# Kernel tuning notes

Hardware: AMD Instinct MI355X
Metric: run time of the kernel (lower is better)

## Reference

```python
import jax, jax.numpy as jnp
import numpy as np
from jax import lax

B, C, H, W = 64, 256, 64, 64
RED = 16


def setup_inputs() -> dict:
    key = jax.random.key(0)
    k1, k2, k3, k4, k5 = jax.random.split(key, 5)
    x = jax.random.normal(k1, (B, C, H, W), dtype=jnp.float32)
    # conv1: Conv2d(C, 1, kernel_size=1) -> weight (1,C,1,1) stored squeezed as (C,), bias scalar
    conv_w = jax.random.normal(k2, (C,), dtype=jnp.float32) * (1.0 / np.sqrt(C))
    conv_b = jax.random.normal(k3, (1,), dtype=jnp.float32) * 0.01
    # SE MLP: Linear(C, C//RED, bias=False), Linear(C//RED, C, bias=False)
    fc1_w = jax.random.normal(k4, (C // RED, C), dtype=jnp.float32) * (1.0 / np.sqrt(C))
    fc2_w = jax.random.normal(k5, (C, C // RED), dtype=jnp.float32) * (1.0 / np.sqrt(C // RED))
    return {"x": x, "conv_w": conv_w, "conv_b": conv_b, "fc1_w": fc1_w, "fc2_w": fc2_w}


def reference(x, conv_w, conv_b, fc1_w, fc2_w):
    b, c, h, w = x.shape
    # --- spatial_pool ---
    # group batch into chunks of 8, pool over (group, H, W) with 3x3x3 avg, stride 1, pad 1
    g = x.reshape(b // 8, 8, c, h, w).transpose(0, 2, 1, 3, 4)  # (G, C, 8, H, W)
    summed = lax.reduce_window(
        g, 0.0, lax.add,
        window_dimensions=(1, 1, 3, 3, 3),
        window_strides=(1, 1, 1, 1, 1),
        padding=[(0, 0), (0, 0), (1, 1), (1, 1), (1, 1)],
    )
    pooled = summed / 27.0  # AvgPool3d(3,1,1) with count_include_pad=True
    pooled = pooled.transpose(0, 2, 1, 3, 4).reshape(b, c, h, w)
    # 1x1 conv C -> 1
    logits = jnp.einsum('bchw,c->bhw', pooled, conv_w) + conv_b[0]  # (B,H,W)
    attn = jax.nn.softmax(logits.reshape(b, h * w), axis=-1)  # softmax over spatial positions
    # softmax-weighted spatial pooling of the ORIGINAL x
    y = jnp.einsum('bcs,bs->bc', x.reshape(b, c, h * w), attn)  # (B,C)
    # --- SE gating MLP ---
    hid = jax.nn.relu(y @ fc1_w.T)           # (B, C//RED)
    gate = jax.nn.sigmoid(hid @ fc2_w.T)     # (B, C)
    return x * gate[:, :, None, None]
```

## Files before the change

### kernel.cpp

```cpp
#include <hip/hip_runtime.h>
#include <math.h>

#define B 64
#define C 256
#define S 4096
#define S4 1024

__global__ __launch_bounds__(256) void k1_chanreduce(const float4* __restrict__ x4,
                                                     const float* __restrict__ cw,
                                                     float4* __restrict__ t4) {
    __shared__ float wl[C];
    const int tid = threadIdx.x;
    wl[tid] = cw[tid];
    __syncthreads();
    const int b = blockIdx.x >> 2;
    const int chunk = blockIdx.x & 3;
    const int s4 = chunk * 256 + tid;
    const float4* xb = x4 + (size_t)b * C * S4 + s4;
    float4 acc = make_float4(0.f, 0.f, 0.f, 0.f);
#pragma unroll 8
    for (int c = 0; c < C; ++c) {
        float4 v = xb[(size_t)c * S4];
        float w = wl[c];
        acc.x += v.x * w; acc.y += v.y * w; acc.z += v.z * w; acc.w += v.w * w;
    }
    t4[b * S4 + s4] = acc;
}

__global__ __launch_bounds__(256) void k2_pool_softmax(const float* __restrict__ t,
                                                       const float* __restrict__ cb,
                                                       float* __restrict__ attn) {
    __shared__ float ts[S];
    __shared__ float rs[S];
    __shared__ float red[16];
    const int b = blockIdx.x;
    const int d = b & 7;
    const int tid = threadIdx.x;
    const float* t0 = t + (size_t)b * S;

    for (int k = 0; k < 16; ++k) {
        int s = k * 256 + tid;
        float v = t0[s];
        if (d > 0) v += t0[s - S];
        if (d < 7) v += t0[s + S];
        ts[s] = v;
    }
    __syncthreads();
    for (int k = 0; k < 16; ++k) {
        int s = k * 256 + tid;
        int w = s & 63;
        float v = ts[s];
        if (w > 0)  v += ts[s - 1];
        if (w < 63) v += ts[s + 1];
        rs[s] = v;
    }
    __syncthreads();
    const float bias = cb[0];
    float l[16];
    float m = -INFINITY;
    for (int k = 0; k < 16; ++k) {
        int s = k * 256 + tid;
        float v = rs[s];
        if (s >= 64)     v += rs[s - 64];
        if (s < S - 64)  v += rs[s + 64];
        l[k] = v * (1.0f / 27.0f) + bias;
        m = fmaxf(m, l[k]);
    }
    for (int o = 32; o > 0; o >>= 1) m = fmaxf(m, __shfl_xor(m, o));
    const int wave = tid >> 6;
    if ((tid & 63) == 0) red[wave] = m;
    __syncthreads();
    if (tid == 0) {
        float mm = red[0];
        for (int i = 1; i < 4; ++i) mm = fmaxf(mm, red[i]);
        red[8] = mm;
    }
    __syncthreads();
    m = red[8];
    float sum = 0.f;
    for (int k = 0; k < 16; ++k) { l[k] = expf(l[k] - m); sum += l[k]; }
    for (int o = 32; o > 0; o >>= 1) sum += __shfl_xor(sum, o);
    if ((tid & 63) == 0) red[wave] = sum;
    __syncthreads();
    if (tid == 0) {
        float ss = red[0] + red[1] + red[2] + red[3];
        red[9] = 1.0f / ss;
    }
    __syncthreads();
    const float inv = red[9];
    float* ab = attn + (size_t)b * S;
    for (int k = 0; k < 16; ++k) {
        int s = k * 256 + tid;
        ab[s] = l[k] * inv;
    }
}

__global__ __launch_bounds__(256) void k3_weighted_pool(const float4* __restrict__ x4,
                                                        const float4* __restrict__ attn4,
                                                        float* __restrict__ y) {
    __shared__ float4 al[S4];
    const int tid = threadIdx.x;
    const int b = blockIdx.x >> 6;
    const int cg = blockIdx.x & 63;
    for (int k = 0; k < 4; ++k) {
        int i = k * 256 + tid;
        al[i] = attn4[(size_t)b * S4 + i];
    }
    __syncthreads();
    const int c = cg * 4 + (tid >> 6);
    const int lane = tid & 63;
    const float4* xb = x4 + ((size_t)(b * C + c)) * S4;
    float acc = 0.f;
#pragma unroll 4
    for (int it = 0; it < 16; ++it) {
        int s4 = it * 64 + lane;
        float4 xv = xb[s4];
        float4 av = al[s4];
        acc += xv.x * av.x + xv.y * av.y + xv.z * av.z + xv.w * av.w;
    }
    for (int o = 32; o > 0; o >>= 1) acc += __shfl_xor(acc, o);
    if (lane == 0) y[b * C + c] = acc;
}

__global__ __launch_bounds__(256) void k4_mlp(const float* __restrict__ y,
                                              const float* __restrict__ fc1,
                                              const float* __restrict__ fc2,
                                              float* __restrict__ gate) {
    __shared__ float yl[C];
    __shared__ float ph[16][17];
    __shared__ float hid[16];
    const int b = blockIdx.x;
    const int tid = threadIdx.x;
    yl[tid] = y[(size_t)b * C + tid];
    __syncthreads();
    const int j = tid >> 4, part = tid & 15;
    float p = 0.f;
#pragma unroll
    for (int k = 0; k < 16; ++k) {
        int cc = part + k * 16;
        p += yl[cc] * fc1[j * C + cc];
    }
    ph[j][part] = p;
    __syncthreads();
    if (tid < 16) {
        float s = 0.f;
#pragma unroll
        for (int k = 0; k < 16; ++k) s += ph[tid][k];
        hid[tid] = fmaxf(s, 0.f);
    }
    __syncthreads();
    float g = 0.f;
#pragma unroll
    for (int jj = 0; jj < 16; ++jj) g += hid[jj] * fc2[tid * 16 + jj];
    gate[(size_t)b * C + tid] = 1.0f / (1.0f + expf(-g));
}

__global__ __launch_bounds__(256) void k5_scale(const float4* __restrict__ x4,
                                               const float* __restrict__ gate,
                                               float4* __restrict__ out4) {
    const size_t total = (size_t)B * C * S4;
    size_t i = (size_t)blockIdx.x * 256 + threadIdx.x;
    const size_t stride = (size_t)gridDim.x * 256;
    for (; i < total; i += stride) {
        int bc = (int)(i >> 10);
        float g = gate[bc];
        float4 v = x4[i];
        v.x *= g; v.y *= g; v.z *= g; v.w *= g;
        out4[i] = v;
    }
}

extern "C" void kernel_launch(void* const* d_in, const int* in_sizes, int n_in,
                              void* d_out, int out_size, void* d_ws, size_t ws_size,
                              hipStream_t stream) {
    const float* x   = (const float*)d_in[0];
    const float* cw  = (const float*)d_in[1];
    const float* cb  = (const float*)d_in[2];
    const float* fc1 = (const float*)d_in[3];
    const float* fc2 = (const float*)d_in[4];
    float* out = (float*)d_out;

    float* t    = (float*)d_ws;
    float* attn = t + (size_t)B * S;
    float* y    = attn + (size_t)B * S;
    float* gate = y + (size_t)B * C;

    k1_chanreduce<<<256, 256, 0, stream>>>((const float4*)x, cw, (float4*)t);
    k2_pool_softmax<<<B, 256, 0, stream>>>(t, cb, attn);
    k3_weighted_pool<<<B * 64, 256, 0, stream>>>((const float4*)x, (const float4*)attn, y);
    k4_mlp<<<B, 256, 0, stream>>>(y, fc1, fc2, gate);
    k5_scale<<<4096, 256, 0, stream>>>((const float4*)x, gate, (float4*)out);
}
```

Before: 546.7 us.

## Fuse SE MLP into scale kernel, split channel reduce, reverse k3 batch order

The channel-reduction kernel now runs 1024 blocks: four waves each reduce 64 channels and the partial sums are combined through shared memory. The weighted-pool kernel drops its shared-memory staging of attention and walks batches in reverse order, presumably to hit data k2/k1 left in cache. The SE MLP is fused into the scale kernel, so each of 1024 blocks recomputes the gate for its batch, and x/out use nontemporal loads and stores. This removes one launch and the gate round trip, and adds occupancy to k1. In exchange the MLP work is repeated 16 times per batch.

Result: faster. 533.8 us (-2.4%).

```diff
diff --git a/kernel.cpp b/kernel.cpp
--- a/kernel.cpp
+++ b/kernel.cpp
@@ -6,25 +6,37 @@
 #define S 4096
 #define S4 1024
 
+typedef float v4f __attribute__((ext_vector_type(4)));
+
 __global__ __launch_bounds__(256) void k1_chanreduce(const float4* __restrict__ x4,
                                                      const float* __restrict__ cw,
                                                      float4* __restrict__ t4) {
-    __shared__ float wl[C];
-    const int tid = threadIdx.x;
-    wl[tid] = cw[tid];
-    __syncthreads();
-    const int b = blockIdx.x >> 2;
-    const int chunk = blockIdx.x & 3;
-    const int s4 = chunk * 256 + tid;
-    const float4* xb = x4 + (size_t)b * C * S4 + s4;
+    __shared__ float4 sh[256];
+    const int tid = threadIdx.x;
+    const int b = blockIdx.x >> 4;
+    const int chunk = blockIdx.x & 15;
+    const int cg = tid >> 6;
+    const int s4i = tid & 63;
+    const int s4 = chunk * 64 + s4i;
+    const float4* xb = x4 + (size_t)b * C * S4 + (size_t)cg * 64 * S4 + s4;
     float4 acc = make_float4(0.f, 0.f, 0.f, 0.f);
 #pragma unroll 8
-    for (int c = 0; c < C; ++c) {
-        float4 v = xb[(size_t)c * S4];
-        float w = wl[c];
+    for (int k = 0; k < 64; ++k) {
+        float4 v = xb[(size_t)k * S4];
+        float w = cw[cg * 64 + k];
         acc.x += v.x * w; acc.y += v.y * w; acc.z += v.z * w; acc.w += v.w * w;
     }
-    t4[b * S4 + s4] = acc;
+    sh[tid] = acc;
+    __syncthreads();
+    if (cg == 0) {
+        float4 a = sh[s4i], b2 = sh[64 + s4i], c2 = sh[128 + s4i], d2 = sh[192 + s4i];
+        float4 r;
+        r.x = a.x + b2.x + c2.x + d2.x;
+        r.y = a.y + b2.y + c2.y + d2.y;
+        r.z = a.z + b2.z + c2.z + d2.z;
+        r.w = a.w + b2.w + c2.w + d2.w;
+        t4[(size_t)b * S4 + s4] = r;
+    }
 }
 
 __global__ __launch_bounds__(256) void k2_pool_softmax(const float* __restrict__ t,
@@ -98,49 +110,51 @@
 __global__ __launch_bounds__(256) void k3_weighted_pool(const float4* __restrict__ x4,
                                                         const float4* __restrict__ attn4,
                                                         float* __restrict__ y) {
-    __shared__ float4 al[S4];
-    const int tid = threadIdx.x;
-    const int b = blockIdx.x >> 6;
+    const int tid = threadIdx.x;
+    const int b = (B - 1) - (blockIdx.x >> 6);
     const int cg = blockIdx.x & 63;
-    for (int k = 0; k < 4; ++k) {
-        int i = k * 256 + tid;
-        al[i] = attn4[(size_t)b * S4 + i];
-    }
-    __syncthreads();
     const int c = cg * 4 + (tid >> 6);
     const int lane = tid & 63;
     const float4* xb = x4 + ((size_t)(b * C + c)) * S4;
+    const float4* ab = attn4 + (size_t)b * S4;
     float acc = 0.f;
 #pragma unroll 4
     for (int it = 0; it < 16; ++it) {
         int s4 = it * 64 + lane;
         float4 xv = xb[s4];
-        float4 av = al[s4];
+        float4 av = ab[s4];
         acc += xv.x * av.x + xv.y * av.y + xv.z * av.z + xv.w * av.w;
     }
+#pragma unroll
     for (int o = 32; o > 0; o >>= 1) acc += __shfl_xor(acc, o);
     if (lane == 0) y[b * C + c] = acc;
 }
 
-__global__ __launch_bounds__(256) void k4_mlp(const float* __restrict__ y,
-                                              const float* __restrict__ fc1,
-                                              const float* __restrict__ fc2,
-                                              float* __restrict__ gate) {
+__global__ __launch_bounds__(256) void k5_mlp_scale(const v4f* __restrict__ x4,
+                                                    const float* __restrict__ y,
+                                                    const float* __restrict__ fc1,
+                                                    const float* __restrict__ fc2,
+                                                    v4f* __restrict__ out4) {
     __shared__ float yl[C];
     __shared__ float ph[16][17];
     __shared__ float hid[16];
-    const int b = blockIdx.x;
-    const int tid = threadIdx.x;
+    __shared__ float gl[C];
+    const int tid = threadIdx.x;
+    const int b = blockIdx.x >> 4;
+    const int chunk = blockIdx.x & 15;
+
     yl[tid] = y[(size_t)b * C + tid];
     __syncthreads();
-    const int j = tid >> 4, part = tid & 15;
-    float p = 0.f;
-#pragma unroll
-    for (int k = 0; k < 16; ++k) {
-        int cc = part + k * 16;
-        p += yl[cc] * fc1[j * C + cc];
-    }
-    ph[j][part] = p;
+    {
+        const int j = tid >> 4, part = tid & 15;
+        float p = 0.f;
+#pragma unroll
+        for (int k = 0; k < 16; ++k) {
+            int cc = part + k * 16;
+            p += yl[cc] * fc1[j * C + cc];
+        }
+        ph[j][part] = p;
+    }
     __syncthreads();
     if (tid < 16) {
         float s = 0.f;
@@ -149,24 +163,25 @@
         hid[tid] = fmaxf(s, 0.f);
     }
     __syncthreads();
-    float g = 0.f;
-#pragma unroll
-    for (int jj = 0; jj < 16; ++jj) g += hid[jj] * fc2[tid * 16 + jj];
-    gate[(size_t)b * C + tid] = 1.0f / (1.0f + expf(-g));
-}
-
-__global__ __launch_bounds__(256) void k5_scale(const float4* __restrict__ x4,
-                                               const float* __restrict__ gate,
-                                               float4* __restrict__ out4) {
-    const size_t total = (size_t)B * C * S4;
-    size_t i = (size_t)blockIdx.x * 256 + threadIdx.x;
-    const size_t stride = (size_t)gridDim.x * 256;
-    for (; i < total; i += stride) {
-        int bc = (int)(i >> 10);
-        float g = gate[bc];
-        float4 v = x4[i];
-        v.x *= g; v.y *= g; v.z *= g; v.w *= g;
-        out4[i] = v;
+    {
+        float g = 0.f;
+#pragma unroll
+        for (int jj = 0; jj < 16; ++jj) g += hid[jj] * fc2[tid * 16 + jj];
+        gl[tid] = 1.0f / (1.0f + expf(-g));
+    }
+    __syncthreads();
+
+    const int s4i = tid & 63;
+    const int cw_ = tid >> 6;
+    const size_t base = (size_t)b * C * S4 + (size_t)chunk * 64 + s4i;
+#pragma unroll 4
+    for (int it = 0; it < 64; ++it) {
+        int ch = it * 4 + cw_;
+        float g = gl[ch];
+        size_t idx = base + (size_t)ch * S4;
+        v4f v = __builtin_nontemporal_load(&x4[idx]);
+        v *= g;
+        __builtin_nontemporal_store(v, &out4[idx]);
     }
 }
 
@@ -183,11 +198,9 @@
     float* t    = (float*)d_ws;
     float* attn = t + (size_t)B * S;
     float* y    = attn + (size_t)B * S;
-    float* gate = y + (size_t)B * C;
-
-    k1_chanreduce<<<256, 256, 0, stream>>>((const float4*)x, cw, (float4*)t);
+
+    k1_chanreduce<<<B * 16, 256, 0, stream>>>((const float4*)x, cw, (float4*)t);
     k2_pool_softmax<<<B, 256, 0, stream>>>(t, cb, attn);
     k3_weighted_pool<<<B * 64, 256, 0, stream>>>((const float4*)x, (const float4*)attn, y);
-    k4_mlp<<<B, 256, 0, stream>>>(y, fc1, fc2, gate);
-    k5_scale<<<4096, 256, 0, stream>>>((const float4*)x, gate, (float4*)out);
-}
+    k5_mlp_scale<<<B * 16, 256, 0, stream>>>((const v4f*)x, y, fc1, fc2, (v4f*)out);
+}
```
